# Performance work log

Hardware: AMD Instinct MI355X
Metric: run time of the kernel (lower is better)

The kernel has to match this reference:

```python
import jax, jax.numpy as jnp
import numpy as np

D_MODEL = 512
NUM_HEADS = 8
D_FF = 2048
SEQ = 2048
BATCH = 2
EPS = 1e-5


def _linear(x, W, b):
    # x: [S,B,D_in], W: [D_out, D_in] (torch convention), b: [D_out]
    return jnp.einsum('sbd,ed->sbe', x, W) + b


def _layer_norm(x, g, b):
    mu = jnp.mean(x, axis=-1, keepdims=True)
    var = jnp.var(x, axis=-1, keepdims=True)
    return (x - mu) * jax.lax.rsqrt(var + EPS) * g + b


def _mha(q_in, k_in, v_in, W, b, mask4d, num_heads):
    # q_in: [Sq,B,D], k_in/v_in: [Sk,B,D]; W: [4,D,D], b: [4,D]
    Sq, B, D = q_in.shape
    Sk = k_in.shape[0]
    dk = D // num_heads
    q = _linear(q_in, W[0], b[0]).reshape(Sq, B, num_heads, dk).transpose(1, 2, 0, 3)
    k = _linear(k_in, W[1], b[1]).reshape(Sk, B, num_heads, dk).transpose(1, 2, 0, 3)
    v = _linear(v_in, W[2], b[2]).reshape(Sk, B, num_heads, dk).transpose(1, 2, 0, 3)
    scores = jnp.einsum('bhqd,bhkd->bhqk', q, k) / jnp.sqrt(jnp.asarray(dk, q.dtype))
    scores = jnp.where(mask4d, -jnp.inf, scores)
    p = jax.nn.softmax(scores, axis=-1)  # dropout p=0 -> identity
    o = jnp.einsum('bhqk,bhkd->bhqd', p, v)  # [B,H,Sq,dk]
    o = o.transpose(2, 0, 1, 3).reshape(Sq, B, D)
    return _linear(o, W[3], b[3])


def setup_inputs() -> dict:
    key = jax.random.key(0)
    ks = jax.random.split(key, 12)
    scale = 1.0 / np.sqrt(D_MODEL)
    inp = {
        'x': jax.random.normal(ks[0], (SEQ, BATCH, D_MODEL), jnp.float32),
        'memory': jax.random.normal(ks[1], (SEQ, BATCH, D_MODEL), jnp.float32),
        # causal mask: True = masked (strictly upper triangular)
        'tgt_mask': jnp.triu(jnp.ones((SEQ, SEQ), dtype=bool), k=1),
        # per-batch key padding mask for cross attention
        'memory_mask': jax.random.randint(ks[2], (BATCH, SEQ), 0, 2) > 0,
        'sa_W': jax.random.normal(ks[3], (4, D_MODEL, D_MODEL), jnp.float32) * scale,
        'sa_b': jnp.zeros((4, D_MODEL), jnp.float32),
        'ca_W': jax.random.normal(ks[4], (4, D_MODEL, D_MODEL), jnp.float32) * scale,
        'ca_b': jnp.zeros((4, D_MODEL), jnp.float32),
        'w1': jax.random.normal(ks[5], (D_FF, D_MODEL), jnp.float32) * scale,
        'b1': jnp.zeros((D_FF,), jnp.float32),
        'w2': jax.random.normal(ks[6], (D_MODEL, D_FF), jnp.float32) * (1.0 / np.sqrt(D_FF)),
        'b2': jnp.zeros((D_MODEL,), jnp.float32),
        'ln_g': jnp.ones((3, D_MODEL), jnp.float32),
        'ln_b': jnp.zeros((3, D_MODEL), jnp.float32),
    }
    return inp


def reference(x, memory, tgt_mask, memory_mask, sa_W, sa_b, ca_W, ca_b,
              w1, b1, w2, b2, ln_g, ln_b):
    # self-attention block (pre-norm, residual)
    nx = _layer_norm(x, ln_g[0], ln_b[0])
    sa = _mha(nx, nx, nx, sa_W, sa_b, tgt_mask[None, None], NUM_HEADS)
    x = x + sa
    # cross-attention block
    nx = _layer_norm(x, ln_g[1], ln_b[1])
    ca = _mha(nx, memory, memory, ca_W, ca_b, memory_mask[:, None, None, :], NUM_HEADS)
    x = x + ca
    # FFN block
    nx = _layer_norm(x, ln_g[2], ln_b[2])
    ff = _linear(jax.nn.relu(_linear(nx, w1, b1)), w2, b2)
    return x + ff
```

## Files before the change

### kernel.cpp

```cpp
#include <hip/hip_runtime.h>

#define S_LEN 2048
#define BATCH_N 2
#define DM 512
#define H_N 8
#define DK_N 64
#define FF_N 2048
#define M_TOK (S_LEN*BATCH_N)
#define QSZ (BATCH_N*H_N*S_LEN*DK_N)

typedef __attribute__((ext_vector_type(8))) short short8;
typedef __attribute__((ext_vector_type(4))) float f32x4;
typedef __attribute__((ext_vector_type(16))) float f32x16;
typedef __attribute__((ext_vector_type(4))) unsigned uint4v;

__device__ __forceinline__ unsigned short f2b(float f) {
  union { float f; unsigned u; } v; v.f = f;
  unsigned r = v.u + 0x7FFFu + ((v.u >> 16) & 1u);
  return (unsigned short)(r >> 16);
}
__device__ __forceinline__ float b2f(unsigned short u) {
  union { unsigned u; float f; } v; v.u = ((unsigned)u) << 16; return v.f;
}

__device__ __forceinline__ void gl_lds16(const void* g, void* l) {
  __builtin_amdgcn_global_load_lds(
      (__attribute__((address_space(1))) unsigned int*)(unsigned long long)g,
      (__attribute__((address_space(3))) unsigned int*)(unsigned int)(unsigned long long)l,
      16, 0, 0);
}

__device__ __forceinline__ void cast4(const float* __restrict__ src,
                                      unsigned short* __restrict__ dst, int i) {
  float4 v = *(const float4*)(src + i);
  ushort4 o; o.x = f2b(v.x); o.y = f2b(v.y); o.z = f2b(v.z); o.w = f2b(v.w);
  *(ushort4*)(dst + i) = o;
}

__global__ __launch_bounds__(256) void prep_kernel(
    const float* __restrict__ sa_W, const float* __restrict__ ca_W,
    const float* __restrict__ w1, const float* __restrict__ w2,
    const float* __restrict__ memory, const int* __restrict__ mm,
    unsigned short* __restrict__ o_sa, unsigned short* __restrict__ o_ca,
    unsigned short* __restrict__ o_w1, unsigned short* __restrict__ o_w2,
    unsigned short* __restrict__ o_mem, unsigned long long* __restrict__ bmo)
{
  int blk = blockIdx.x, t = threadIdx.x;
  if (blk < 1024)      cast4(sa_W, o_sa, (blk*256 + t)*4);
  else if (blk < 2048) cast4(ca_W, o_ca, ((blk-1024)*256 + t)*4);
  else if (blk < 3072) cast4(w1,   o_w1, ((blk-2048)*256 + t)*4);
  else if (blk < 4096) cast4(w2,   o_w2, ((blk-3072)*256 + t)*4);
  else if (blk < 6144) cast4(memory, o_mem, ((blk-4096)*256 + t)*4);
  else if (t < 64) {
    int b = t >> 5, kt = t & 31;
    unsigned long long m = 0ull;
    for (int j = 0; j < 64; j++)
      m |= (unsigned long long)(mm[b*S_LEN + kt*64 + j] != 0) << j;
    bmo[b*32 + kt] = m;
  }
}

__global__ __launch_bounds__(128) void ln_kernel(const float* __restrict__ in,
                                                 const float* __restrict__ g,
                                                 const float* __restrict__ b,
                                                 unsigned short* __restrict__ out) {
  int row = blockIdx.x, t = threadIdx.x;
  float4 v = ((const float4*)(in + (size_t)row * DM))[t];
  float s  = v.x + v.y + v.z + v.w;
  float ss = v.x*v.x + v.y*v.y + v.z*v.z + v.w*v.w;
  #pragma unroll
  for (int off = 32; off >= 1; off >>= 1) {
    s  += __shfl_xor(s,  off);
    ss += __shfl_xor(ss, off);
  }
  __shared__ float sh[4];
  if ((t & 63) == 0) { sh[(t>>6)*2] = s; sh[(t>>6)*2+1] = ss; }
  __syncthreads();
  s = sh[0] + sh[2]; ss = sh[1] + sh[3];
  float mean = s * (1.f/512.f);
  float inv  = rsqrtf(ss * (1.f/512.f) - mean*mean + 1e-5f);
  float4 gv = ((const float4*)g)[t];
  float4 bv = ((const float4*)b)[t];
  ushort4 o;
  o.x = f2b((v.x-mean)*inv*gv.x + bv.x);
  o.y = f2b((v.y-mean)*inv*gv.y + bv.y);
  o.z = f2b((v.z-mean)*inv*gv.z + bv.z);
  o.w = f2b((v.w-mean)*inv*gv.w + bv.w);
  ((ushort4*)out)[(size_t)row*128 + t] = o;
}

template<int RELU, int OUTMODE, int RESID>
__global__ __launch_bounds__(256) void gemm_bt(
    const unsigned short* __restrict__ A, const unsigned short* __restrict__ W,
    const float* __restrict__ bias, const float* __restrict__ resid,
    float* __restrict__ Cf, unsigned short* __restrict__ Cb,
    int M, int N, int K)
{
  __shared__ unsigned short As[2][64*40];
  __shared__ unsigned short Bs[2][64*40];
  int tid = threadIdx.x;
  int lane = tid & 63, w = tid >> 6;
  int wr = w >> 1, wc = w & 1;
  int bm = blockIdx.y * 64, bn = blockIdx.x * 64;
  f32x4 acc[2][2] = {};
  int lrow = tid >> 2;
  int lcg  = (tid & 3) * 8;
  const size_t aoff = (size_t)(bm + lrow) * K + lcg;
  const size_t boff = (size_t)(bn + lrow) * K + lcg;
  int fr = lane & 15, kg = (lane >> 4) * 8;
  short8 pa = *(const short8*)&A[aoff];
  short8 pb = *(const short8*)&W[boff];
  *(short8*)&As[0][lrow*40 + lcg] = pa;
  *(short8*)&Bs[0][lrow*40 + lcg] = pb;
  __syncthreads();
  int cur = 0;
  for (int k0 = 0; k0 < K; k0 += 32) {
    bool hn = (k0 + 32) < K;
    if (hn) {
      pa = *(const short8*)&A[aoff + k0 + 32];
      pb = *(const short8*)&W[boff + k0 + 32];
    }
    short8 af0 = *(const short8*)&As[cur][(wr*32 +      fr)*40 + kg];
    short8 af1 = *(const short8*)&As[cur][(wr*32 + 16 + fr)*40 + kg];
    short8 bf0 = *(const short8*)&Bs[cur][(wc*32 +      fr)*40 + kg];
    short8 bf1 = *(const short8*)&Bs[cur][(wc*32 + 16 + fr)*40 + kg];
    acc[0][0] = __builtin_amdgcn_mfma_f32_16x16x32_bf16(af0, bf0, acc[0][0], 0,0,0);
    acc[0][1] = __builtin_amdgcn_mfma_f32_16x16x32_bf16(af0, bf1, acc[0][1], 0,0,0);
    acc[1][0] = __builtin_amdgcn_mfma_f32_16x16x32_bf16(af1, bf0, acc[1][0], 0,0,0);
    acc[1][1] = __builtin_amdgcn_mfma_f32_16x16x32_bf16(af1, bf1, acc[1][1], 0,0,0);
    if (hn) {
      *(short8*)&As[cur^1][lrow*40 + lcg] = pa;
      *(short8*)&Bs[cur^1][lrow*40 + lcg] = pb;
    }
    __syncthreads();
    cur ^= 1;
  }
  int rbase = (lane >> 4) * 4;
  #pragma unroll
  for (int m = 0; m < 2; m++) {
    #pragma unroll
    for (int n = 0; n < 2; n++) {
      int col = bn + wc*32 + n*16 + (lane & 15);
      float bc = bias[col];
      #pragma unroll
      for (int r = 0; r < 4; r++) {
        int row = bm + wr*32 + m*16 + rbase + r;
        float vv = acc[m][n][r] + bc;
        if (RELU) vv = fmaxf(vv, 0.f);
        if (OUTMODE == 2) {
          int which = col >> 9, hh = (col >> 6) & 7, dd = col & 63;
          size_t idx = ((((size_t)which*BATCH_N + (row & 1))*H_N + hh)*S_LEN + (row >> 1))*DK_N + dd;
          Cb[idx] = f2b(vv);
        } else {
          size_t idx = (size_t)row * N + col;
          if (RESID) vv += resid[idx];
          if (OUTMODE == 1) Cb[idx] = f2b(vv);
          else              Cf[idx] = vv;
        }
      }
    }
  }
}

template<int RELU, int OUTMODE, int VSTART>
__global__ __launch_bounds__(256) void gemm128(
    const unsigned short* __restrict__ A, const unsigned short* __restrict__ W,
    const float* __restrict__ bias, unsigned short* __restrict__ Cb,
    int M, int N, int K)
{
  __shared__ unsigned short As[128*32];
  __shared__ unsigned short Bs[128*32];
  int tid = threadIdx.x, lane = tid & 63, w = tid >> 6;
  int bm = blockIdx.y * 128, bn = blockIdx.x * 128;
  int fr = lane & 15, hi = lane >> 4;
  int kg8 = hi*8, rg = hi*4;
  int wm = (w >> 1) * 64, wn = (w & 1) * 64;
  f32x4 acc[4][4] = {};
  const unsigned short* ga0 = A + (size_t)(bm +      (tid>>2))*K + (tid&3)*8;
  const unsigned short* ga1 = A + (size_t)(bm + 64 + (tid>>2))*K + (tid&3)*8;
  const unsigned short* gb0 = W + (size_t)(bn +      (tid>>2))*K + (tid&3)*8;
  const unsigned short* gb1 = W + (size_t)(bn + 64 + (tid>>2))*K + (tid&3)*8;
  unsigned short* lA0 = &As[tid*8];
  unsigned short* lA1 = &As[2048 + tid*8];
  unsigned short* lB0 = &Bs[tid*8];
  unsigned short* lB1 = &Bs[2048 + tid*8];
  for (int k0 = 0; k0 < K; k0 += 32) {
    gl_lds16(ga0 + k0, lA0);
    gl_lds16(ga1 + k0, lA1);
    gl_lds16(gb0 + k0, lB0);
    gl_lds16(gb1 + k0, lB1);
    __syncthreads();
    short8 af[4], bf[4];
    #pragma unroll
    for (int m = 0; m < 4; m++) af[m] = *(const short8*)&As[(wm + m*16 + fr)*32 + kg8];
    #pragma unroll
    for (int n = 0; n < 4; n++) bf[n] = *(const short8*)&Bs[(wn + n*16 + fr)*32 + kg8];
    __builtin_amdgcn_s_setprio(1);
    #pragma unroll
    for (int m = 0; m < 4; m++)
      #pragma unroll
      for (int n = 0; n < 4; n++)
        acc[m][n] = __builtin_amdgcn_mfma_f32_16x16x32_bf16(af[m], bf[n], acc[m][n], 0,0,0);
    __builtin_amdgcn_s_setprio(0);
    __syncthreads();
  }
  #pragma unroll
  for (int m = 0; m < 4; m++) {
    #pragma unroll
    for (int n = 0; n < 4; n++) {
      int col = bn + wn + n*16 + fr;
      float bc = bias[col];
      #pragma unroll
      for (int r = 0; r < 4; r++) {
        int row = bm + wm + m*16 + rg + r;
        float vv = acc[m][n][r] + bc;
        if (RELU) vv = fmaxf(vv, 0.f);
        if (OUTMODE == 2) {
          int which = col >> 9, hh = (col >> 6) & 7, dd = col & 63;
          int srow = row >> 1, bb = row & 1;
          size_t idx;
          if (which >= VSTART)
            idx = (size_t)which*QSZ + (((size_t)bb*H_N + hh)*DK_N + dd)*S_LEN + srow;
          else
            idx = (size_t)which*QSZ + (((size_t)bb*H_N + hh)*S_LEN + srow)*DK_N + dd;
          Cb[idx] = f2b(vv);
        } else {
          Cb[(size_t)row * N + col] = f2b(vv);
        }
      }
    }
  }
}

template<int MODE>
__global__ __launch_bounds__(256, 3) void attn3(
    const unsigned short* __restrict__ qg, const unsigned short* __restrict__ kpl,
    const unsigned short* __restrict__ vtpl, const unsigned long long* __restrict__ bm,
    unsigned short* __restrict__ opart, float* __restrict__ lpart)
{
  __shared__ unsigned short SM[2*64*72];
  unsigned short* Ks = SM;
  unsigned short* Vt = SM + 64*72;
  int tid = threadIdx.x;
  int lane = tid & 63, w = tid >> 6;
  int l31 = lane & 31, hi5 = lane >> 5;
  int bid = blockIdx.x;
  int p = bid & 15, u = bid >> 4;
  int qtile = u >> 2, range = u & 3;
  int h = p & 7, b = p >> 3;
  const size_t sbase = (size_t)(b*H_N + h) * S_LEN;
  int kt0 = range*8, kt1 = kt0 + 7;
  if (MODE == 0) {
    int ktmax_tile = qtile*2 + 1;
    if (kt0 > ktmax_tile) {
      int zr = tid >> 1, zc = (tid & 1) * 32;
      short8 z = {};
      size_t zb = (size_t)range*QSZ + (sbase + (size_t)qtile*128 + zr)*DK_N + zc;
      *(short8*)&opart[zb]      = z;
      *(short8*)&opart[zb + 8]  = z;
      *(short8*)&opart[zb + 16] = z;
      *(short8*)&opart[zb + 24] = z;
      if (tid < 128) lpart[range*32768 + (int)sbase + qtile*128 + tid] = 0.f;
      return;
    }
    if (kt1 > ktmax_tile) kt1 = ktmax_tile;
  }
  int qrow = qtile*128 + w*32 + l31;
  short8 qf[4];
  #pragma unroll
  for (int km = 0; km < 4; km++)
    qf[km] = *(const short8*)&qg[(sbase + qrow)*DK_N + km*16 + hi5*8];

  int sr = tid >> 2, sc = (tid & 3) * 16;
  const unsigned short* kbase = &kpl[(sbase + sr)*DK_N + sc];
  const unsigned short* vbase = &vtpl[((size_t)(b*H_N + h)*DK_N + sr)*S_LEN + sc];

  f32x16 oa0 = {}, oa1 = {};
  float lp = 0.f;
  for (int kt = kt0; kt <= kt1; kt++) {
    __syncthreads();
    {
      const unsigned short* kg = kbase + (size_t)kt*64*DK_N;
      const unsigned short* vg = vbase + kt*64;
      *(short8*)&Ks[sr*72 + sc]     = *(const short8*)kg;
      *(short8*)&Ks[sr*72 + sc + 8] = *(const short8*)(kg + 8);
      *(short8*)&Vt[sr*72 + sc]     = *(const short8*)vg;
      *(short8*)&Vt[sr*72 + sc + 8] = *(const short8*)(vg + 8);
    }
    __syncthreads();
    #pragma unroll
    for (int kb = 0; kb < 2; kb++) {
      f32x16 sa = {};
      __builtin_amdgcn_s_setprio(1);
      #pragma unroll
      for (int km = 0; km < 4; km++) {
        short8 kf = *(const short8*)&Ks[(kb*32 + l31)*72 + km*16 + hi5*8];
        sa = __builtin_amdgcn_mfma_f32_32x32x16_bf16(kf, qf[km], sa, 0, 0, 0);
      }
      __builtin_amdgcn_s_setprio(0);
      unsigned mlo = 0;
      if (MODE == 1) mlo = (unsigned)(bm[b*32 + kt] >> (kb*32 + 4*hi5));
      float pv[16];
      float psum = 0.f;
      #pragma unroll
      for (int r = 0; r < 16; r++) {
        const int pos = (r & 3) + 8*(r >> 2);
        float e = __expf(sa[r] * 0.125f);
        bool dead;
        if (MODE == 0) dead = (kt*64 + kb*32 + 4*hi5 + pos) > qrow;
        else           dead = ((mlo >> pos) & 1u) != 0u;
        e = dead ? 0.f : e;
        pv[r] = e;
        psum += e;
      }
      lp += psum;
      unsigned pk[8];
      #pragma unroll
      for (int i = 0; i < 8; i++)
        asm("v_cvt_pk_bf16_f32 %0, %1, %2" : "=v"(pk[i]) : "v"(pv[2*i]), "v"(pv[2*i+1]));
      asm("v_permlane32_swap_b32 %0, %1" : "+v"(pk[0]), "+v"(pk[2]));
      asm("v_permlane32_swap_b32 %0, %1" : "+v"(pk[1]), "+v"(pk[3]));
      asm("v_permlane32_swap_b32 %0, %1" : "+v"(pk[4]), "+v"(pk[6]));
      asm("v_permlane32_swap_b32 %0, %1" : "+v"(pk[5]), "+v"(pk[7]));
      uint4v f0v, f1v;
      f0v.x = pk[0]; f0v.y = pk[1]; f0v.z = pk[2]; f0v.w = pk[3];
      f1v.x = pk[4]; f1v.y = pk[5]; f1v.z = pk[6]; f1v.w = pk[7];
      short8 pf0 = *(short8*)&f0v;
      short8 pf1 = *(short8*)&f1v;
      __builtin_amdgcn_s_setprio(1);
      {
        short8 v00 = *(const short8*)&Vt[(     l31)*72 + kb*32 +      hi5*8];
        short8 v01 = *(const short8*)&Vt[(     l31)*72 + kb*32 + 16 + hi5*8];
        oa0 = __builtin_amdgcn_mfma_f32_32x32x16_bf16(pf0, v00, oa0, 0, 0, 0);
        oa0 = __builtin_amdgcn_mfma_f32_32x32x16_bf16(pf1, v01, oa0, 0, 0, 0);
        short8 v10 = *(const short8*)&Vt[(32 + l31)*72 + kb*32 +      hi5*8];
        short8 v11 = *(const short8*)&Vt[(32 + l31)*72 + kb*32 + 16 + hi5*8];
        oa1 = __builtin_amdgcn_mfma_f32_32x32x16_bf16(pf0, v10, oa1, 0, 0, 0);
        oa1 = __builtin_amdgcn_mfma_f32_32x32x16_bf16(pf1, v11, oa1, 0, 0, 0);
      }
      __builtin_amdgcn_s_setprio(0);
    }
  }
  float lptot = lp + __shfl_xor(lp, 32);
  if (lane < 32)
    lpart[range*32768 + (int)sbase + qtile*128 + w*32 + l31] = lptot;
  #pragma unroll
  for (int r = 0; r < 16; r++) {
    const int pos = (r & 3) + 8*(r >> 2);
    int qr = qtile*128 + w*32 + pos + 4*hi5;
    size_t obase = (size_t)range*QSZ + (sbase + (size_t)qr)*DK_N;
    opart[obase + l31]      = f2b(oa0[r]);
    opart[obase + 32 + l31] = f2b(oa1[r]);
  }
}

__global__ __launch_bounds__(256) void attn_combine4(
    const unsigned short* __restrict__ op, const float* __restrict__ lp,
    unsigned short* __restrict__ o)
{
  int t = blockIdx.x*256 + threadIdx.x;
  int f = t*8;
  int col = f & 511, row = f >> 9;
  int h = col >> 6, d = col & 63, s = row >> 1, b = row & 1;
  size_t pr = ((size_t)b*H_N + h)*S_LEN + s;
  size_t base = pr*DK_N + d;
  float acc[8] = {0.f,0.f,0.f,0.f,0.f,0.f,0.f,0.f};
  float l = 0.f;
  #pragma unroll
  for (int r = 0; r < 4; r++) {
    short8 a = *(const short8*)&op[(size_t)r*QSZ + base];
    #pragma unroll
    for (int i = 0; i < 8; i++) acc[i] += b2f((unsigned short)a[i]);
    l += lp[r*32768 + (int)pr];
  }
  float inv = 1.f / l;
  short8 r8;
  #pragma unroll
  for (int i = 0; i < 8; i++) r8[i] = (short)f2b(acc[i] * inv);
  *(short8*)&o[(size_t)row*DM + col] = r8;
}

extern "C" void kernel_launch(void* const* d_in, const int* in_sizes, int n_in,
                              void* d_out, int out_size, void* d_ws, size_t ws_size,
                              hipStream_t stream) {
  const float* x       = (const float*)d_in[0];
  const float* memory  = (const float*)d_in[1];
  const int*   memmask = (const int*)d_in[3];
  const float* sa_W = (const float*)d_in[4];
  const float* sa_b = (const float*)d_in[5];
  const float* ca_W = (const float*)d_in[6];
  const float* ca_b = (const float*)d_in[7];
  const float* w1   = (const float*)d_in[8];
  const float* b1   = (const float*)d_in[9];
  const float* w2   = (const float*)d_in[10];
  const float* b2   = (const float*)d_in[11];
  const float* ln_g = (const float*)d_in[12];
  const float* ln_b = (const float*)d_in[13];
  float* out = (float*)d_out;

  char* ws = (char*)d_ws;
  float*          xcur   = (float*)ws;
  unsigned short* nx_bf  = (unsigned short*)(ws + (8u<<20));
  unsigned short* qkv_sa = (unsigned short*)(ws + (12u<<20));
  unsigned short* q_ca   = (unsigned short*)(ws + (24u<<20));
  unsigned short* kv_ca  = (unsigned short*)(ws + (28u<<20));
  unsigned short* o_bf   = (unsigned short*)(ws + (36u<<20));
  unsigned short* mem_bf = (unsigned short*)(ws + (40u<<20));
  unsigned short* h_bf   = (unsigned short*)(ws + (44u<<20));
  unsigned short* opart  = (unsigned short*)(ws + (44u<<20));
  float*          lpart  = (float*)(ws + (60u<<20));
  unsigned long long* bmsk = (unsigned long long*)(ws + (60u<<20) + (1u<<19));
  unsigned short* w_sa   = (unsigned short*)(ws + (61u<<20));
  unsigned short* w_ca   = w_sa + 4*512*512;
  unsigned short* w_f1   = w_ca + 4*512*512;
  unsigned short* w_f2   = w_f1 + 2048*512;

  prep_kernel<<<6145, 256, 0, stream>>>(sa_W, ca_W, w1, w2, memory, memmask,
                                        w_sa, w_ca, w_f1, w_f2, mem_bf, bmsk);

  dim3 blk(256);
  dim3 g512 (512/64,  4096/64);
  dim3 q128_1536(1536/128, 4096/128);
  dim3 q128_1024(1024/128, 4096/128);
  dim3 q128_2048(2048/128, 4096/128);

  ln_kernel<<<4096, 128, 0, stream>>>(x, ln_g, ln_b, nx_bf);
  gemm128<0,2,2><<<q128_1536, blk, 0, stream>>>(nx_bf, w_sa, sa_b, qkv_sa, 4096, 1536, 512);
  attn3<0><<<1024, 256, 0, stream>>>(qkv_sa, qkv_sa + QSZ, qkv_sa + 2*QSZ, nullptr, opart, lpart);
  attn_combine4<<<1024, 256, 0, stream>>>(opart, lpart, o_bf);
  gemm_bt<0,0,1><<<g512, blk, 0, stream>>>(o_bf, w_sa + 3*262144, sa_b + 1536, x, xcur, nullptr, 4096, 512, 512);

  ln_kernel<<<4096, 128, 0, stream>>>(xcur, ln_g + 512, ln_b + 512, nx_bf);
  gemm_bt<0,2,0><<<g512, blk, 0, stream>>>(nx_bf, w_ca, ca_b, nullptr, nullptr, q_ca, 4096, 512, 512);
  gemm128<0,2,1><<<q128_1024, blk, 0, stream>>>(mem_bf, w_ca + 262144, ca_b + 512, kv_ca, 4096, 1024, 512);
  attn3<1><<<1024, 256, 0, stream>>>(q_ca, kv_ca, kv_ca + QSZ, bmsk, opart, lpart);
  attn_combine4<<<1024, 256, 0, stream>>>(opart, lpart, o_bf);
  gemm_bt<0,0,1><<<g512, blk, 0, stream>>>(o_bf, w_ca + 3*262144, ca_b + 1536, xcur, xcur, nullptr, 4096, 512, 512);

  ln_kernel<<<4096, 128, 0, stream>>>(xcur, ln_g + 1024, ln_b + 1024, nx_bf);
  gemm128<1,1,0><<<q128_2048, blk, 0, stream>>>(nx_bf, w_f1, b1, h_bf, 4096, 2048, 512);
  gemm_bt<0,0,1><<<g512, blk, 0, stream>>>(h_bf, w_f2, b2, xcur, out, nullptr, 4096, 512, 2048);
}
```

Baseline: 208.7 us.

## Fuse first LayerNorm into prep, merge QKV GEMMs, split-K FFN2, wave-per-row LN

The first LayerNorm moves into the prep kernel, and the self-attention QKV projection and cross-attention KV projection run as a single dual GEMM launch. LayerNorm now uses one wave per row with no shared-memory reduction. The FFN down-projection (K=2048) becomes a 4-way split-K GEMM with a separate combine kernel that adds bias and residual. Attention occupancy is raised to 4 blocks per SM. The goal is fewer launches and more parallelism in the long-K GEMM, at the cost of extra fp32 partial traffic and higher register pressure in attention.

```diff
diff --git a/kernel.cpp b/kernel.cpp
--- a/kernel.cpp
+++ b/kernel.cpp
@@ -8,6 +8,7 @@
 #define FF_N 2048
 #define M_TOK (S_LEN*BATCH_N)
 #define QSZ (BATCH_N*H_N*S_LEN*DK_N)
+#define MN_PART 2097152
 
 typedef __attribute__((ext_vector_type(8))) short short8;
 typedef __attribute__((ext_vector_type(4))) float f32x4;
@@ -37,13 +38,47 @@
   *(ushort4*)(dst + i) = o;
 }
 
+__device__ __forceinline__ void ln_row_wave(const float* __restrict__ in,
+    const float* __restrict__ g, const float* __restrict__ b,
+    unsigned short* __restrict__ out, int row, int lane) {
+  const float4* src = (const float4*)(in + (size_t)row * DM);
+  float4 v0 = src[lane*2], v1 = src[lane*2 + 1];
+  float s  = v0.x+v0.y+v0.z+v0.w + v1.x+v1.y+v1.z+v1.w;
+  float ss = v0.x*v0.x+v0.y*v0.y+v0.z*v0.z+v0.w*v0.w
+           + v1.x*v1.x+v1.y*v1.y+v1.z*v1.z+v1.w*v1.w;
+  #pragma unroll
+  for (int off = 32; off >= 1; off >>= 1) {
+    s  += __shfl_xor(s,  off);
+    ss += __shfl_xor(ss, off);
+  }
+  float mean = s * (1.f/512.f);
+  float inv  = rsqrtf(ss * (1.f/512.f) - mean*mean + 1e-5f);
+  float4 g0 = ((const float4*)g)[lane*2], g1 = ((const float4*)g)[lane*2 + 1];
+  float4 b0 = ((const float4*)b)[lane*2], b1 = ((const float4*)b)[lane*2 + 1];
+  ushort4 o0, o1;
+  o0.x = f2b((v0.x-mean)*inv*g0.x + b0.x);
+  o0.y = f2b((v0.y-mean)*inv*g0.y + b0.y);
+  o0.z = f2b((v0.z-mean)*inv*g0.z + b0.z);
+  o0.w = f2b((v0.w-mean)*inv*g0.w + b0.w);
+  o1.x = f2b((v1.x-mean)*inv*g1.x + b1.x);
+  o1.y = f2b((v1.y-mean)*inv*g1.y + b1.y);
+  o1.z = f2b((v1.z-mean)*inv*g1.z + b1.z);
+  o1.w = f2b((v1.w-mean)*inv*g1.w + b1.w);
+  ushort4* dst = (ushort4*)(out + (size_t)row * DM);
+  dst[lane*2]     = o0;
+  dst[lane*2 + 1] = o1;
+}
+
 __global__ __launch_bounds__(256) void prep_kernel(
     const float* __restrict__ sa_W, const float* __restrict__ ca_W,
     const float* __restrict__ w1, const float* __restrict__ w2,
     const float* __restrict__ memory, const int* __restrict__ mm,
+    const float* __restrict__ x, const float* __restrict__ ln_g,
+    const float* __restrict__ ln_b,
     unsigned short* __restrict__ o_sa, unsigned short* __restrict__ o_ca,
     unsigned short* __restrict__ o_w1, unsigned short* __restrict__ o_w2,
-    unsigned short* __restrict__ o_mem, unsigned long long* __restrict__ bmo)
+    unsigned short* __restrict__ o_mem, unsigned long long* __restrict__ bmo,
+    unsigned short* __restrict__ nx)
 {
   int blk = blockIdx.x, t = threadIdx.x;
   if (blk < 1024)      cast4(sa_W, o_sa, (blk*256 + t)*4);
@@ -51,42 +86,25 @@
   else if (blk < 3072) cast4(w1,   o_w1, ((blk-2048)*256 + t)*4);
   else if (blk < 4096) cast4(w2,   o_w2, ((blk-3072)*256 + t)*4);
   else if (blk < 6144) cast4(memory, o_mem, ((blk-4096)*256 + t)*4);
-  else if (t < 64) {
-    int b = t >> 5, kt = t & 31;
-    unsigned long long m = 0ull;
-    for (int j = 0; j < 64; j++)
-      m |= (unsigned long long)(mm[b*S_LEN + kt*64 + j] != 0) << j;
-    bmo[b*32 + kt] = m;
-  }
-}
-
-__global__ __launch_bounds__(128) void ln_kernel(const float* __restrict__ in,
-                                                 const float* __restrict__ g,
-                                                 const float* __restrict__ b,
-                                                 unsigned short* __restrict__ out) {
-  int row = blockIdx.x, t = threadIdx.x;
-  float4 v = ((const float4*)(in + (size_t)row * DM))[t];
-  float s  = v.x + v.y + v.z + v.w;
-  float ss = v.x*v.x + v.y*v.y + v.z*v.z + v.w*v.w;
-  #pragma unroll
-  for (int off = 32; off >= 1; off >>= 1) {
-    s  += __shfl_xor(s,  off);
-    ss += __shfl_xor(ss, off);
-  }
-  __shared__ float sh[4];
-  if ((t & 63) == 0) { sh[(t>>6)*2] = s; sh[(t>>6)*2+1] = ss; }
-  __syncthreads();
-  s = sh[0] + sh[2]; ss = sh[1] + sh[3];
-  float mean = s * (1.f/512.f);
-  float inv  = rsqrtf(ss * (1.f/512.f) - mean*mean + 1e-5f);
-  float4 gv = ((const float4*)g)[t];
-  float4 bv = ((const float4*)b)[t];
-  ushort4 o;
-  o.x = f2b((v.x-mean)*inv*gv.x + bv.x);
-  o.y = f2b((v.y-mean)*inv*gv.y + bv.y);
-  o.z = f2b((v.z-mean)*inv*gv.z + bv.z);
-  o.w = f2b((v.w-mean)*inv*gv.w + bv.w);
-  ((ushort4*)out)[(size_t)row*128 + t] = o;
+  else if (blk == 6144) {
+    if (t < 64) {
+      int b = t >> 5, kt = t & 31;
+      unsigned long long m = 0ull;
+      for (int j = 0; j < 64; j++)
+        m |= (unsigned long long)(mm[b*S_LEN + kt*64 + j] != 0) << j;
+      bmo[b*32 + kt] = m;
+    }
+  } else {
+    int row = (blk - 6145)*4 + (t >> 6);
+    ln_row_wave(x, ln_g, ln_b, nx, row, t & 63);
+  }
+}
+
+__global__ __launch_bounds__(256) void ln4_kernel(const float* __restrict__ in,
+                                                  const float* __restrict__ g,
+                                                  const float* __restrict__ b,
+                                                  unsigned short* __restrict__ out) {
+  ln_row_wave(in, g, b, out, blockIdx.x*4 + (threadIdx.x >> 6), threadIdx.x & 63);
 }
 
 template<int RELU, int OUTMODE, int RESID>
@@ -94,7 +112,7 @@
     const unsigned short* __restrict__ A, const unsigned short* __restrict__ W,
     const float* __restrict__ bias, const float* __restrict__ resid,
     float* __restrict__ Cf, unsigned short* __restrict__ Cb,
-    int M, int N, int K)
+    int M, int N, int K, int Kstride)
 {
   __shared__ unsigned short As[2][64*40];
   __shared__ unsigned short Bs[2][64*40];
@@ -102,11 +120,12 @@
   int lane = tid & 63, w = tid >> 6;
   int wr = w >> 1, wc = w & 1;
   int bm = blockIdx.y * 64, bn = blockIdx.x * 64;
+  int kz = blockIdx.z;
   f32x4 acc[2][2] = {};
   int lrow = tid >> 2;
   int lcg  = (tid & 3) * 8;
-  const size_t aoff = (size_t)(bm + lrow) * K + lcg;
-  const size_t boff = (size_t)(bn + lrow) * K + lcg;
+  const size_t aoff = (size_t)(bm + lrow) * Kstride + (size_t)kz * K + lcg;
+  const size_t boff = (size_t)(bn + lrow) * Kstride + (size_t)kz * K + lcg;
   int fr = lane & 15, kg = (lane >> 4) * 8;
   short8 pa = *(const short8*)&A[aoff];
   short8 pb = *(const short8*)&W[boff];
@@ -141,7 +160,7 @@
     #pragma unroll
     for (int n = 0; n < 2; n++) {
       int col = bn + wc*32 + n*16 + (lane & 15);
-      float bc = bias[col];
+      float bc = (OUTMODE == 3) ? 0.f : bias[col];
       #pragma unroll
       for (int r = 0; r < 4; r++) {
         int row = bm + wr*32 + m*16 + rbase + r;
@@ -151,6 +170,8 @@
           int which = col >> 9, hh = (col >> 6) & 7, dd = col & 63;
           size_t idx = ((((size_t)which*BATCH_N + (row & 1))*H_N + hh)*S_LEN + (row >> 1))*DK_N + dd;
           Cb[idx] = f2b(vv);
+        } else if (OUTMODE == 3) {
+          Cf[(size_t)kz*MN_PART + (size_t)row*N + col] = vv;
         } else {
           size_t idx = (size_t)row * N + col;
           if (RESID) vv += resid[idx];
@@ -160,6 +181,25 @@
       }
     }
   }
+}
+
+__global__ __launch_bounds__(256) void ffn2_combine(
+    const float* __restrict__ part, const float* __restrict__ bias,
+    const float* __restrict__ resid, float* __restrict__ out)
+{
+  int i = (blockIdx.x*256 + threadIdx.x)*4;
+  float4 a = *(const float4*)(part + i);
+  float4 b = *(const float4*)(part + MN_PART + i);
+  float4 c = *(const float4*)(part + 2*MN_PART + i);
+  float4 d = *(const float4*)(part + 3*MN_PART + i);
+  float4 bs = *(const float4*)(bias + (i & 511));
+  float4 rs = *(const float4*)(resid + i);
+  float4 o;
+  o.x = a.x + b.x + c.x + d.x + bs.x + rs.x;
+  o.y = a.y + b.y + c.y + d.y + bs.y + rs.y;
+  o.z = a.z + b.z + c.z + d.z + bs.z + rs.z;
+  o.w = a.w + b.w + c.w + d.w + bs.w + rs.w;
+  *(float4*)(out + i) = o;
 }
 
 template<int RELU, int OUTMODE, int VSTART>
@@ -232,8 +272,79 @@
   }
 }
 
+__global__ __launch_bounds__(256) void gemm128_dual(
+    const unsigned short* __restrict__ A0, const unsigned short* __restrict__ W0,
+    const float* __restrict__ bias0, unsigned short* __restrict__ C0,
+    const unsigned short* __restrict__ A1, const unsigned short* __restrict__ W1,
+    const float* __restrict__ bias1, unsigned short* __restrict__ C1)
+{
+  const int K = 512;
+  int bx = blockIdx.x;
+  const unsigned short* A; const unsigned short* W; const float* bias;
+  unsigned short* Cb; int bn, vs;
+  if (bx < 12) { A = A0; W = W0; bias = bias0; Cb = C0; bn = bx*128;      vs = 2; }
+  else         { A = A1; W = W1; bias = bias1; Cb = C1; bn = (bx-12)*128; vs = 1; }
+  __shared__ unsigned short As[128*32];
+  __shared__ unsigned short Bs[128*32];
+  int tid = threadIdx.x, lane = tid & 63, w = tid >> 6;
+  int bm = blockIdx.y * 128;
+  int fr = lane & 15, hi = lane >> 4;
+  int kg8 = hi*8, rg = hi*4;
+  int wm = (w >> 1) * 64, wn = (w & 1) * 64;
+  f32x4 acc[4][4] = {};
+  const unsigned short* ga0 = A + (size_t)(bm +      (tid>>2))*K + (tid&3)*8;
+  const unsigned short* ga1 = A + (size_t)(bm + 64 + (tid>>2))*K + (tid&3)*8;
+  const unsigned short* gb0 = W + (size_t)(bn +      (tid>>2))*K + (tid&3)*8;
+  const unsigned short* gb1 = W + (size_t)(bn + 64 + (tid>>2))*K + (tid&3)*8;
+  unsigned short* lA0 = &As[tid*8];
+  unsigned short* lA1 = &As[2048 + tid*8];
+  unsigned short* lB0 = &Bs[tid*8];
+  unsigned short* lB1 = &Bs[2048 + tid*8];
+  for (int k0 = 0; k0 < K; k0 += 32) {
+    gl_lds16(ga0 + k0, lA0);
+    gl_lds16(ga1 + k0, lA1);
+    gl_lds16(gb0 + k0, lB0);
+    gl_lds16(gb1 + k0, lB1);
+    __syncthreads();
+    short8 af[4], bf[4];
+    #pragma unroll
+    for (int m = 0; m < 4; m++) af[m] = *(const short8*)&As[(wm + m*16 + fr)*32 + kg8];
+    #pragma unroll
+    for (int n = 0; n < 4; n++) bf[n] = *(const short8*)&Bs[(wn + n*16 + fr)*32 + kg8];
+    __builtin_amdgcn_s_setprio(1);
+    #pragma unroll
+    for (int m = 0; m < 4; m++)
+      #pragma unroll
+      for (int n = 0; n < 4; n++)
+        acc[m][n] = __builtin_amdgcn_mfma_f32_16x16x32_bf16(af[m], bf[n], acc[m][n], 0,0,0);
+    __builtin_amdgcn_s_setprio(0);
+    __syncthreads();
+  }
+  #pragma unroll
+  for (int m = 0; m < 4; m++) {
+    #pragma unroll
+    for (int n = 0; n < 4; n++) {
+      int col = bn + wn + n*16 + fr;
+      float bc = bias[col];
+      #pragma unroll
+      for (int r = 0; r < 4; r++) {
+        int row = bm + wm + m*16 + rg + r;
+        float vv = acc[m][n][r] + bc;
+        int which = col >> 9, hh = (col >> 6) & 7, dd = col & 63;
+        int srow = row >> 1, bb = row & 1;
+        size_t idx;
+        if (which >= vs)
+          idx = (size_t)which*QSZ + (((size_t)bb*H_N + hh)*DK_N + dd)*S_LEN + srow;
+        else
+          idx = (size_t)which*QSZ + (((size_t)bb*H_N + hh)*S_LEN + srow)*DK_N + dd;
+        Cb[idx] = f2b(vv);
+      }
+    }
+  }
+}
+
 template<int MODE>
-__global__ __launch_bounds__(256, 3) void attn3(
+__global__ __launch_bounds__(256, 4) void attn3(
     const unsigned short* __restrict__ qg, const unsigned short* __restrict__ kpl,
     const unsigned short* __restrict__ vtpl, const unsigned long long* __restrict__ bm,
     unsigned short* __restrict__ opart, float* __restrict__ lpart)
@@ -408,6 +519,7 @@
   unsigned short* mem_bf = (unsigned short*)(ws + (40u<<20));
   unsigned short* h_bf   = (unsigned short*)(ws + (44u<<20));
   unsigned short* opart  = (unsigned short*)(ws + (44u<<20));
+  float*          fpart  = (float*)(ws + (12u<<20));
   float*          lpart  = (float*)(ws + (60u<<20));
   unsigned long long* bmsk = (unsigned long long*)(ws + (60u<<20) + (1u<<19));
   unsigned short* w_sa   = (unsigned short*)(ws + (61u<<20));
@@ -415,29 +527,30 @@
   unsigned short* w_f1   = w_ca + 4*512*512;
   unsigned short* w_f2   = w_f1 + 2048*512;
 
-  prep_kernel<<<6145, 256, 0, stream>>>(sa_W, ca_W, w1, w2, memory, memmask,
-                                        w_sa, w_ca, w_f1, w_f2, mem_bf, bmsk);
-
   dim3 blk(256);
   dim3 g512 (512/64,  4096/64);
-  dim3 q128_1536(1536/128, 4096/128);
-  dim3 q128_1024(1024/128, 4096/128);
+  dim3 gdual(20, 4096/128);
   dim3 q128_2048(2048/128, 4096/128);
-
-  ln_kernel<<<4096, 128, 0, stream>>>(x, ln_g, ln_b, nx_bf);
-  gemm128<0,2,2><<<q128_1536, blk, 0, stream>>>(nx_bf, w_sa, sa_b, qkv_sa, 4096, 1536, 512);
-  attn3<0><<<1024, 256, 0, stream>>>(qkv_sa, qkv_sa + QSZ, qkv_sa + 2*QSZ, nullptr, opart, lpart);
-  attn_combine4<<<1024, 256, 0, stream>>>(opart, lpart, o_bf);
-  gemm_bt<0,0,1><<<g512, blk, 0, stream>>>(o_bf, w_sa + 3*262144, sa_b + 1536, x, xcur, nullptr, 4096, 512, 512);
-
-  ln_kernel<<<4096, 128, 0, stream>>>(xcur, ln_g + 512, ln_b + 512, nx_bf);
-  gemm_bt<0,2,0><<<g512, blk, 0, stream>>>(nx_bf, w_ca, ca_b, nullptr, nullptr, q_ca, 4096, 512, 512);
-  gemm128<0,2,1><<<q128_1024, blk, 0, stream>>>(mem_bf, w_ca + 262144, ca_b + 512, kv_ca, 4096, 1024, 512);
-  attn3<1><<<1024, 256, 0, stream>>>(q_ca, kv_ca, kv_ca + QSZ, bmsk, opart, lpart);
-  attn_combine4<<<1024, 256, 0, stream>>>(opart, lpart, o_bf);
-  gemm_bt<0,0,1><<<g512, blk, 0, stream>>>(o_bf, w_ca + 3*262144, ca_b + 1536, xcur, xcur, nullptr, 4096, 512, 512);
-
-  ln_kernel<<<4096, 128, 0, stream>>>(xcur, ln_g + 1024, ln_b + 1024, nx_bf);
+  dim3 gsplitk(512/64, 4096/64, 4);
+
+  prep_kernel<<<7169, blk, 0, stream>>>(sa_W, ca_W, w1, w2, memory, memmask,
+                                        x, ln_g, ln_b,
+                                        w_sa, w_ca, w_f1, w_f2, mem_bf, bmsk, nx_bf);
+
+  gemm128_dual<<<gdual, blk, 0, stream>>>(nx_bf, w_sa, sa_b, qkv_sa,
+                                          mem_bf, w_ca + 262144, ca_b + 512, kv_ca);
+  attn3<0><<<1024, blk, 0, stream>>>(qkv_sa, qkv_sa + QSZ, qkv_sa + 2*QSZ, nullptr, opart, lpart);
+  attn_combine4<<<1024, blk, 0, stream>>>(opart, lpart, o_bf);
+  gemm_bt<0,0,1><<<g512, blk, 0, stream>>>(o_bf, w_sa + 3*262144, sa_b + 1536, x, xcur, nullptr, 4096, 512, 512, 512);
+
+  ln4_kernel<<<1024, blk, 0, stream>>>(xcur, ln_g + 512, ln_b + 512, nx_bf);
+  gemm_bt<0,2,0><<<g512, blk, 0, stream>>>(nx_bf, w_ca, ca_b, nullptr, nullptr, q_ca, 4096, 512, 512, 512);
+  attn3<1><<<1024, blk, 0, stream>>>(q_ca, kv_ca, kv_ca + QSZ, bmsk, opart, lpart);
+  attn_combine4<<<1024, blk, 0, stream>>>(opart, lpart, o_bf);
+  gemm_bt<0,0,1><<<g512, blk, 0, stream>>>(o_bf, w_ca + 3*262144, ca_b + 1536, xcur, xcur, nullptr, 4096, 512, 512, 512);
+
+  ln4_kernel<<<1024, blk, 0, stream>>>(xcur, ln_g + 1024, ln_b + 1024, nx_bf);
   gemm128<1,1,0><<<q128_2048, blk, 0, stream>>>(nx_bf, w_f1, b1, h_bf, 4096, 2048, 512);
-  gemm_bt<0,0,1><<<g512, blk, 0, stream>>>(h_bf, w_f2, b2, xcur, out, nullptr, 4096, 512, 2048);
-}
+  gemm_bt<0,3,0><<<gsplitk, blk, 0, stream>>>(h_bf, w_f2, nullptr, nullptr, fpart, nullptr, 4096, 512, 512, 2048);
+  ffn2_combine<<<2048, blk, 0, stream>>>(fpart, b2, xcur, out);
+}
```

Measured after the change: 201.6 us. -3.4%, faster.
